# Kernel optimization log

Hardware: AMD Instinct MI355X
Metric: run time of the kernel (lower is better)

## Reference

```python
import jax, jax.numpy as jnp
import numpy as np

D_IN = 4096
UNITS = 4096
NNZ = 262144
BATCH = 1024


def setup_inputs() -> dict:
    key = jax.random.key(0)
    k1, k2, k3, k4, k5 = jax.random.split(key, 5)
    x = jax.random.normal(k1, (BATCH, D_IN), dtype=jnp.float32)
    # trainable sparse kernel values (scaled so outputs stay O(1))
    values = jax.random.normal(k2, (NNZ,), dtype=jnp.float32) * (1.0 / np.sqrt(NNZ / UNITS))
    bias = jax.random.normal(k3, (UNITS,), dtype=jnp.float32) * 0.1
    rows = jax.random.randint(k4, (NNZ,), 0, D_IN, dtype=jnp.int32)
    cols = jax.random.randint(k5, (NNZ,), 0, UNITS, dtype=jnp.int32)
    return {"x": x, "values": values, "bias": bias, "rows": rows, "cols": cols}


def reference(x, values, bias, rows, cols):
    # sparse COO matmul: out[b, c] = sum_{k: cols[k]==c} x[b, rows[k]] * values[k]
    # gather rows of x^T -> [nnz, B], scale by values, scatter-add into columns
    contrib = x.T[rows] * values[:, None]                      # [nnz, B]
    out = jax.ops.segment_sum(contrib, cols, num_segments=UNITS).T  # [B, units]
    out = out + bias[None, :]
    return jax.nn.relu(out)
```

## Files before the change

kernel.cpp:

```cpp
#include <hip/hip_runtime.h>
#include <hip/hip_bf16.h>

#define D_IN  4096
#define UNITS 4096
#define NNZ   262144
#define BATCH 1024
#define CAP   256
#define QB    256
#define NQ    4


__global__ void scatter_kernel(const int* __restrict__ rows,
                               const int* __restrict__ cols,
                               const float* __restrict__ values,
                               int* __restrict__ counts,
                               int2* __restrict__ buckets) {
    int k = blockIdx.x * blockDim.x + threadIdx.x;
    if (k >= NNZ) return;
    int c = cols[k];
    int pos = atomicAdd(&counts[c], 1);
    if (pos < CAP) {
        int2 e;
        e.x = rows[k];
        e.y = __float_as_int(values[k]);
        buckets[c * CAP + pos] = e;
    }
}


__global__ void transpose_x_kernel(const float* __restrict__ x,
                                   unsigned short* __restrict__ xT4) {
    __shared__ float tile[32][33];
    const int nr = D_IN / 32;
    int r0 = (blockIdx.x % nr) * 32;
    int b0 = (blockIdx.x / nr) * 32;
    int tx = threadIdx.x & 31, ty = threadIdx.x >> 5;
    #pragma unroll
    for (int i = 0; i < 32; i += 8)
        tile[ty + i][tx] = x[(size_t)(b0 + ty + i) * D_IN + r0 + tx];
    __syncthreads();
    int q  = b0 >> 8;
    int bq = (b0 & 255) + tx;
    #pragma unroll
    for (int i = 0; i < 32; i += 8) {
        unsigned bits = __float_as_uint(tile[tx][ty + i]);
        unsigned r = (bits + 0x7FFFu + ((bits >> 16) & 1u)) >> 16;
        xT4[((size_t)q * D_IN + (r0 + ty + i)) * QB + bq] = (unsigned short)r;
    }
}


__global__ __launch_bounds__(256) void spmm_kernel(const unsigned short* __restrict__ xT4,
                                                   const int2* __restrict__ buckets,
                                                   const int* __restrict__ counts,
                                                   float* __restrict__ outT) {
    const int bx   = blockIdx.x;
    const int q    = bx >> 10;
    const int cg   = bx & 1023;
    const int wave = __builtin_amdgcn_readfirstlane(threadIdx.x >> 6);
    const int lane = threadIdx.x & 63;
    const int c    = (cg << 2) | wave;

    int n = counts[c];
    if (n > CAP) n = CAP;
    const int2* bk = buckets + (size_t)c * CAP;
    const unsigned short* bp = xT4 + (size_t)q * D_IN * QB + lane * 4;

    float a0 = 0.f, a1 = 0.f, a2 = 0.f, a3 = 0.f;
    int j = 0;
    for (; j + 4 <= n; j += 4) {
        int2 e0 = bk[j + 0];
        int2 e1 = bk[j + 1];
        int2 e2 = bk[j + 2];
        int2 e3 = bk[j + 3];
        uint2 u0 = *(const uint2*)(bp + (size_t)e0.x * QB);
        uint2 u1 = *(const uint2*)(bp + (size_t)e1.x * QB);
        uint2 u2 = *(const uint2*)(bp + (size_t)e2.x * QB);
        uint2 u3 = *(const uint2*)(bp + (size_t)e3.x * QB);
        float v0 = __int_as_float(e0.y), v1 = __int_as_float(e1.y);
        float v2 = __int_as_float(e2.y), v3 = __int_as_float(e3.y);
        a0 += __uint_as_float(u0.x << 16)          * v0;
        a1 += __uint_as_float(u0.x & 0xffff0000u)  * v0;
        a2 += __uint_as_float(u0.y << 16)          * v0;
        a3 += __uint_as_float(u0.y & 0xffff0000u)  * v0;
        a0 += __uint_as_float(u1.x << 16)          * v1;
        a1 += __uint_as_float(u1.x & 0xffff0000u)  * v1;
        a2 += __uint_as_float(u1.y << 16)          * v1;
        a3 += __uint_as_float(u1.y & 0xffff0000u)  * v1;
        a0 += __uint_as_float(u2.x << 16)          * v2;
        a1 += __uint_as_float(u2.x & 0xffff0000u)  * v2;
        a2 += __uint_as_float(u2.y << 16)          * v2;
        a3 += __uint_as_float(u2.y & 0xffff0000u)  * v2;
        a0 += __uint_as_float(u3.x << 16)          * v3;
        a1 += __uint_as_float(u3.x & 0xffff0000u)  * v3;
        a2 += __uint_as_float(u3.y << 16)          * v3;
        a3 += __uint_as_float(u3.y & 0xffff0000u)  * v3;
    }
    for (; j < n; ++j) {
        int2 e = bk[j];
        uint2 u = *(const uint2*)(bp + (size_t)e.x * QB);
        float v = __int_as_float(e.y);
        a0 += __uint_as_float(u.x << 16)          * v;
        a1 += __uint_as_float(u.x & 0xffff0000u)  * v;
        a2 += __uint_as_float(u.y << 16)          * v;
        a3 += __uint_as_float(u.y & 0xffff0000u)  * v;
    }

    float4 r; r.x = a0; r.y = a1; r.z = a2; r.w = a3;
    *(float4*)(outT + (size_t)c * BATCH + q * QB + lane * 4) = r;
}


__global__ void epilogue_kernel(const float* __restrict__ outT,
                                const float* __restrict__ bias,
                                float* __restrict__ out) {
    __shared__ float tile[32][33];
    const int nc = UNITS / 32;
    int c0 = (blockIdx.x % nc) * 32;
    int b0 = (blockIdx.x / nc) * 32;
    int tx = threadIdx.x & 31, ty = threadIdx.x >> 5;
    #pragma unroll
    for (int i = 0; i < 32; i += 8)
        tile[ty + i][tx] = outT[(size_t)(c0 + ty + i) * BATCH + b0 + tx];
    __syncthreads();
    float bv = bias[c0 + tx];
    #pragma unroll
    for (int i = 0; i < 32; i += 8) {
        float v = tile[tx][ty + i] + bv;
        out[(size_t)(b0 + ty + i) * UNITS + c0 + tx] = v > 0.f ? v : 0.f;
    }
}


extern "C" void kernel_launch(void* const* d_in, const int* in_sizes, int n_in,
                              void* d_out, int out_size, void* d_ws, size_t ws_size,
                              hipStream_t stream) {
    const float* x      = (const float*)d_in[0];
    const float* values = (const float*)d_in[1];
    const float* bias   = (const float*)d_in[2];
    const int*   rows   = (const int*)d_in[3];
    const int*   cols   = (const int*)d_in[4];
    float* out = (float*)d_out;

    char* ws = (char*)d_ws;
    unsigned short* xT4 = (unsigned short*)(ws);
    float* outT    = (float*)(ws + (size_t)8 * 1024 * 1024);
    int2*  buckets = (int2*)(ws + (size_t)24 * 1024 * 1024);
    int*   counts  = (int*)(ws + (size_t)32 * 1024 * 1024);

    hipMemsetAsync(counts, 0, UNITS * sizeof(int), stream);

    scatter_kernel<<<(NNZ + 255) / 256, 256, 0, stream>>>(rows, cols, values,
                                                          counts, buckets);

    transpose_x_kernel<<<(D_IN / 32) * (BATCH / 32), 256, 0, stream>>>(x, xT4);

    spmm_kernel<<<NQ * 1024, 256, 0, stream>>>(xT4, buckets, counts, outT);

    epilogue_kernel<<<(UNITS / 32) * (BATCH / 32), 256, 0, stream>>>(outT, bias, out);
}
```

Before: 145.3 us.

## Fuse scatter and transpose kernels; split bucket entries across half-waves with 16B loads

Merges the COO bucket scatter and the x transpose/bf16 conversion into one launch, with block ranges picking the role, so one kernel launch disappears and the two jobs can overlap. In the SpMM kernel each lane now loads 8 bf16 values (16 bytes) instead of 4. The two half-waves handle alternating nonzeros, read from paired uint4 bucket loads, and their partial sums are combined with a cross-half shuffle before store. Block-to-(quarter, column-group) mapping is also reordered so consecutive blocks share buckets across batch quarters. The cost is an extra shuffle reduction and half the lanes idle during the store.

```diff
diff --git a/kernel.cpp b/kernel.cpp
--- a/kernel.cpp
+++ b/kernel.cpp
@@ -9,31 +9,35 @@
 #define QB    256
 #define NQ    4
 
-
-__global__ void scatter_kernel(const int* __restrict__ rows,
-                               const int* __restrict__ cols,
-                               const float* __restrict__ values,
-                               int* __restrict__ counts,
-                               int2* __restrict__ buckets) {
-    int k = blockIdx.x * blockDim.x + threadIdx.x;
-    if (k >= NNZ) return;
-    int c = cols[k];
-    int pos = atomicAdd(&counts[c], 1);
-    if (pos < CAP) {
-        int2 e;
-        e.x = rows[k];
-        e.y = __float_as_int(values[k]);
-        buckets[c * CAP + pos] = e;
-    }
-}
+#define SCAT_BLKS  (NNZ / 256)
+#define TRANS_BLKS ((D_IN / 32) * (BATCH / 32))
 
 
-__global__ void transpose_x_kernel(const float* __restrict__ x,
-                                   unsigned short* __restrict__ xT4) {
+__global__ __launch_bounds__(256) void prep_kernel(const float* __restrict__ x,
+                                                   const int* __restrict__ rows,
+                                                   const int* __restrict__ cols,
+                                                   const float* __restrict__ values,
+                                                   int* __restrict__ counts,
+                                                   int2* __restrict__ buckets,
+                                                   unsigned short* __restrict__ xT4) {
     __shared__ float tile[32][33];
+    int bx = blockIdx.x;
+    if (bx < SCAT_BLKS) {
+        int k = bx * 256 + threadIdx.x;
+        int c = cols[k];
+        int pos = atomicAdd(&counts[c], 1);
+        if (pos < CAP) {
+            int2 e;
+            e.x = rows[k];
+            e.y = __float_as_int(values[k]);
+            buckets[c * CAP + pos] = e;
+        }
+        return;
+    }
+    bx -= SCAT_BLKS;
     const int nr = D_IN / 32;
-    int r0 = (blockIdx.x % nr) * 32;
-    int b0 = (blockIdx.x / nr) * 32;
+    int r0 = (bx % nr) * 32;
+    int b0 = (bx / nr) * 32;
     int tx = threadIdx.x & 31, ty = threadIdx.x >> 5;
     #pragma unroll
     for (int i = 0; i < 32; i += 8)
@@ -50,64 +54,75 @@
 }
 
 
+__device__ __forceinline__ void fma8(float* a, uint4 u, float v) {
+    a[0] += __uint_as_float(u.x << 16)         * v;
+    a[1] += __uint_as_float(u.x & 0xffff0000u) * v;
+    a[2] += __uint_as_float(u.y << 16)         * v;
+    a[3] += __uint_as_float(u.y & 0xffff0000u) * v;
+    a[4] += __uint_as_float(u.z << 16)         * v;
+    a[5] += __uint_as_float(u.z & 0xffff0000u) * v;
+    a[6] += __uint_as_float(u.w << 16)         * v;
+    a[7] += __uint_as_float(u.w & 0xffff0000u) * v;
+}
+
 __global__ __launch_bounds__(256) void spmm_kernel(const unsigned short* __restrict__ xT4,
                                                    const int2* __restrict__ buckets,
                                                    const int* __restrict__ counts,
                                                    float* __restrict__ outT) {
     const int bx   = blockIdx.x;
-    const int q    = bx >> 10;
-    const int cg   = bx & 1023;
+    const int q    = bx & 3;
+    const int cg   = bx >> 2;
     const int wave = __builtin_amdgcn_readfirstlane(threadIdx.x >> 6);
     const int lane = threadIdx.x & 63;
+    const bool hi  = lane >= 32;
     const int c    = (cg << 2) | wave;
 
     int n = counts[c];
     if (n > CAP) n = CAP;
     const int2* bk = buckets + (size_t)c * CAP;
-    const unsigned short* bp = xT4 + (size_t)q * D_IN * QB + lane * 4;
+    const unsigned short* bp = xT4 + (size_t)q * D_IN * QB + (lane & 31) * 8;
 
-    float a0 = 0.f, a1 = 0.f, a2 = 0.f, a3 = 0.f;
+    float a[8];
+    #pragma unroll
+    for (int i = 0; i < 8; ++i) a[i] = 0.f;
+
     int j = 0;
     for (; j + 4 <= n; j += 4) {
-        int2 e0 = bk[j + 0];
-        int2 e1 = bk[j + 1];
-        int2 e2 = bk[j + 2];
-        int2 e3 = bk[j + 3];
-        uint2 u0 = *(const uint2*)(bp + (size_t)e0.x * QB);
-        uint2 u1 = *(const uint2*)(bp + (size_t)e1.x * QB);
-        uint2 u2 = *(const uint2*)(bp + (size_t)e2.x * QB);
-        uint2 u3 = *(const uint2*)(bp + (size_t)e3.x * QB);
-        float v0 = __int_as_float(e0.y), v1 = __int_as_float(e1.y);
-        float v2 = __int_as_float(e2.y), v3 = __int_as_float(e3.y);
-        a0 += __uint_as_float(u0.x << 16)          * v0;
-        a1 += __uint_as_float(u0.x & 0xffff0000u)  * v0;
-        a2 += __uint_as_float(u0.y << 16)          * v0;
-        a3 += __uint_as_float(u0.y & 0xffff0000u)  * v0;
-        a0 += __uint_as_float(u1.x << 16)          * v1;
-        a1 += __uint_as_float(u1.x & 0xffff0000u)  * v1;
-        a2 += __uint_as_float(u1.y << 16)          * v1;
-        a3 += __uint_as_float(u1.y & 0xffff0000u)  * v1;
-        a0 += __uint_as_float(u2.x << 16)          * v2;
-        a1 += __uint_as_float(u2.x & 0xffff0000u)  * v2;
-        a2 += __uint_as_float(u2.y << 16)          * v2;
-        a3 += __uint_as_float(u2.y & 0xffff0000u)  * v2;
-        a0 += __uint_as_float(u3.x << 16)          * v3;
-        a1 += __uint_as_float(u3.x & 0xffff0000u)  * v3;
-        a2 += __uint_as_float(u3.y << 16)          * v3;
-        a3 += __uint_as_float(u3.y & 0xffff0000u)  * v3;
+        uint4 e01 = *(const uint4*)(bk + j);
+        uint4 e23 = *(const uint4*)(bk + j + 2);
+        int   r0 = hi ? (int)e01.z : (int)e01.x;
+        float v0 = hi ? __uint_as_float(e01.w) : __uint_as_float(e01.y);
+        int   r1 = hi ? (int)e23.z : (int)e23.x;
+        float v1 = hi ? __uint_as_float(e23.w) : __uint_as_float(e23.y);
+        uint4 u0 = *(const uint4*)(bp + (size_t)r0 * QB);
+        uint4 u1 = *(const uint4*)(bp + (size_t)r1 * QB);
+        fma8(a, u0, v0);
+        fma8(a, u1, v1);
     }
-    for (; j < n; ++j) {
+    for (; j + 2 <= n; j += 2) {
+        uint4 e01 = *(const uint4*)(bk + j);
+        int   r0 = hi ? (int)e01.z : (int)e01.x;
+        float v0 = hi ? __uint_as_float(e01.w) : __uint_as_float(e01.y);
+        uint4 u0 = *(const uint4*)(bp + (size_t)r0 * QB);
+        fma8(a, u0, v0);
+    }
+    if (j < n) {
         int2 e = bk[j];
-        uint2 u = *(const uint2*)(bp + (size_t)e.x * QB);
-        float v = __int_as_float(e.y);
-        a0 += __uint_as_float(u.x << 16)          * v;
-        a1 += __uint_as_float(u.x & 0xffff0000u)  * v;
-        a2 += __uint_as_float(u.y << 16)          * v;
-        a3 += __uint_as_float(u.y & 0xffff0000u)  * v;
+        float v = hi ? 0.f : __int_as_float(e.y);
+        uint4 u = *(const uint4*)(bp + (size_t)e.x * QB);
+        fma8(a, u, v);
     }
 
-    float4 r; r.x = a0; r.y = a1; r.z = a2; r.w = a3;
-    *(float4*)(outT + (size_t)c * BATCH + q * QB + lane * 4) = r;
+    #pragma unroll
+    for (int i = 0; i < 8; ++i) a[i] += __shfl_xor(a[i], 32, 64);
+
+    if (lane < 32) {
+        float* dst = outT + (size_t)c * BATCH + q * QB + (lane & 31) * 8;
+        float4 r0; r0.x = a[0]; r0.y = a[1]; r0.z = a[2]; r0.w = a[3];
+        float4 r1; r1.x = a[4]; r1.y = a[5]; r1.z = a[6]; r1.w = a[7];
+        *(float4*)dst = r0;
+        *(float4*)(dst + 4) = r1;
+    }
 }
 
 
@@ -150,10 +165,8 @@
 
     hipMemsetAsync(counts, 0, UNITS * sizeof(int), stream);
 
-    scatter_kernel<<<(NNZ + 255) / 256, 256, 0, stream>>>(rows, cols, values,
-                                                          counts, buckets);
-
-    transpose_x_kernel<<<(D_IN / 32) * (BATCH / 32), 256, 0, stream>>>(x, xT4);
+    prep_kernel<<<SCAT_BLKS + TRANS_BLKS, 256, 0, stream>>>(x, rows, cols, values,
+                                                            counts, buckets, xT4);
 
     spmm_kernel<<<NQ * 1024, 256, 0, stream>>>(xT4, buckets, counts, outT);
 
```

Result: faster. 135.1 us (-7.0%).
